# Performance work log

Measured on AMD Instinct MI355X. Metric: run time of the kernel, lower is better.

## Reference

```python
import jax, jax.numpy as jnp
import numpy as np
import math

CHANNELS = 1024
NUM_HEADS = 16
HEAD_DIM = CHANNELS // NUM_HEADS  # 64
ROPE_DIM = int(HEAD_DIM * 0.5)    # 32
BASE_FREQ = 10000.0


def apply_rope(x):
    """x: [b, h, t, d]; rotate first ROPE_DIM features, pass the rest through."""
    t = x.shape[2]
    half = ROPE_DIM // 2
    theta = 1.0 / (BASE_FREQ ** (jnp.arange(0, ROPE_DIM, 2, dtype=jnp.float32) / ROPE_DIM))  # [half]
    ang = jnp.arange(t, dtype=jnp.float32)[:, None] * theta[None, :]  # [t, half]
    ang = jnp.concatenate([ang, ang], axis=-1)  # [t, ROPE_DIM]
    cos = jnp.cos(ang)[None, None, :, :]
    sin = jnp.sin(ang)[None, None, :, :]
    x_rope, x_pass = x[..., :ROPE_DIM], x[..., ROPE_DIM:]
    neg_half = jnp.concatenate([-x_rope[..., half:], x_rope[..., :half]], axis=-1)
    x_rope = x_rope * cos + neg_half * sin
    return jnp.concatenate([x_rope, x_pass], axis=-1)


def proximal_bias(length):
    pos = jnp.arange(length, dtype=jnp.float32)
    diff = pos[None, :] - pos[:, None]
    return -jnp.log1p(jnp.abs(diff))[None, None, :, :]  # [1,1,t,t]


def conv1x1(x, w, b):
    """x: [b, c_in, t], w: [c_out, c_in], b: [c_out] -> [b, c_out, t]"""
    return jnp.einsum('oc,bct->bot', w, x) + b[None, :, None]


def setup_inputs() -> dict:
    key = jax.random.key(0)
    ks = jax.random.split(key, 10)
    B, C, T = 8, CHANNELS, 1024
    scale = 1.0 / math.sqrt(C)
    return {
        "x": jax.random.normal(ks[0], (B, C, T), dtype=jnp.float32),
        "context": jax.random.normal(ks[1], (B, C, T), dtype=jnp.float32),
        "attention_mask": jnp.ones((B, 1, 1, T), dtype=jnp.int32),
        "Wq": jax.random.normal(ks[2], (C, C), dtype=jnp.float32) * scale,
        "bq": jnp.zeros((C,), dtype=jnp.float32),
        "Wk": jax.random.normal(ks[3], (C, C), dtype=jnp.float32) * scale,
        "bk": jnp.zeros((C,), dtype=jnp.float32),
        "Wv": jax.random.normal(ks[4], (C, C), dtype=jnp.float32) * scale,
        "bv": jnp.zeros((C,), dtype=jnp.float32),
        "Wo": jax.random.normal(ks[5], (C, C), dtype=jnp.float32) * scale,
        "bo": jnp.zeros((C,), dtype=jnp.float32),
    }


def reference(x, context, attention_mask, Wq, bq, Wk, bk, Wv, bv, Wo, bo):
    B, C, T = x.shape
    H, D = NUM_HEADS, HEAD_DIM
    q = conv1x1(x, Wq, bq)
    k = conv1x1(context, Wk, bk)
    v = conv1x1(context, Wv, bv)
    # b (h d) t -> b h t d
    def split_heads(z):
        return z.reshape(B, H, D, -1).transpose(0, 1, 3, 2)
    q, k, v = split_heads(q), split_heads(k), split_heads(v)
    q = apply_rope(q)
    k = apply_rope(k)
    scores = jnp.einsum('bhqd,bhkd->bhqk', q, k) / math.sqrt(D)
    scores = scores + proximal_bias(T)  # proximal_bias=True, self-attention
    scores = jnp.where(attention_mask == 0, jnp.float32(-10000.0), scores)
    probs = jax.nn.softmax(scores, axis=-1)  # dropout_rate=0.0 -> identity
    out = jnp.einsum('bhqk,bhkd->bhqd', probs, v)
    # b h q d -> b (h d) q
    out = out.transpose(0, 1, 3, 2).reshape(B, C, T)
    return conv1x1(out, Wo, bo)
```

## Files before the change

kernel.cpp:

```cpp
#include <hip/hip_runtime.h>
#include <hip/hip_bf16.h>
#include <math.h>

#define BB 8
#define CC 1024
#define TT 1024
#define HH 16
#define DD 64

typedef __attribute__((ext_vector_type(8))) short short8;
typedef __attribute__((ext_vector_type(4))) short short4_;
typedef __attribute__((ext_vector_type(4))) float f32x4;

#define QSCALE 0.18033688f

__device__ __forceinline__ unsigned short f2bf(float f) {
    unsigned u = __builtin_bit_cast(unsigned, f);
    u += 0x7fffu + ((u >> 16) & 1u);
    return (unsigned short)(u >> 16);
}

__device__ __forceinline__ f32x4 mfma16(short8 a, short8 b, f32x4 c) {
    return __builtin_amdgcn_mfma_f32_16x16x32_bf16(a, b, c, 0, 0, 0);
}

__device__ __forceinline__ void async16(const void* g, void* l) {
    __builtin_amdgcn_global_load_lds(
        (const __attribute__((address_space(1))) unsigned int*)g,
        (__attribute__((address_space(3))) unsigned int*)l, 16, 0, 0);
}

template<int CTRL>
__device__ __forceinline__ float dpp_mv(float x) {
    return __builtin_bit_cast(float,
        __builtin_amdgcn_update_dpp(0, __builtin_bit_cast(int, x),
                                    CTRL, 0xF, 0xF, false));
}
__device__ __forceinline__ float rowsum16(float x) {
    x += dpp_mv<0xB1>(x);
    x += dpp_mv<0x4E>(x);
    x += dpp_mv<0x141>(x);
    x += dpp_mv<0x140>(x);
    return x;
}

__global__ __launch_bounds__(256) void cast_w_kernel(
    const float* __restrict__ Wq, const float* __restrict__ Wk,
    const float* __restrict__ Wv, const float* __restrict__ Wo,
    unsigned short* __restrict__ dst)
{
    const int z = blockIdx.y;
    const float* W = (z == 0) ? Wq : (z == 1) ? Wk : (z == 2) ? Wv : Wo;
    unsigned short* d = dst + (size_t)z * CC * CC;
    int idx = blockIdx.x * 256 + threadIdx.x;
    float4 f = ((const float4*)W)[idx];
    short4_ s;
    s[0] = (short)f2bf(f.x); s[1] = (short)f2bf(f.y);
    s[2] = (short)f2bf(f.z); s[3] = (short)f2bf(f.w);
    ((short4_*)d)[idx] = s;
}

__global__ __launch_bounds__(256) void tcast2_kernel(
    const float* __restrict__ x, const float* __restrict__ ctx,
    unsigned short* __restrict__ xT, unsigned short* __restrict__ cTo)
{
    __shared__ float sT[64][65];
    const int tid = threadIdx.x;
    const int z = blockIdx.z;
    const float* in = (z < BB) ? x : ctx;
    unsigned short* out = (z < BB) ? xT : cTo;
    const int b = (z < BB) ? z : z - BB;
    const int tB = blockIdx.x * 64, cT = blockIdx.y * 64;

    const float* ib = in + ((size_t)b * CC + cT) * TT + tB;
    const int r = tid >> 2;
    #pragma unroll
    for (int j = 0; j < 4; j++) {
        int t4 = (tid & 3) * 4 + j * 16;
        float4 f = *(const float4*)(ib + (size_t)r * TT + t4);
        sT[r][t4 + 0] = f.x; sT[r][t4 + 1] = f.y;
        sT[r][t4 + 2] = f.z; sT[r][t4 + 3] = f.w;
    }
    __syncthreads();
    const int t_l = tid >> 2, cch = (tid & 3) * 16;
    short8 o0, o1;
    #pragma unroll
    for (int i = 0; i < 8; i++) {
        o0[i] = (short)f2bf(sT[cch + i][t_l]);
        o1[i] = (short)f2bf(sT[cch + 8 + i][t_l]);
    }
    unsigned short* dp = out + ((size_t)b * TT + tB + t_l) * CC + cT + cch;
    *(short8*)dp = o0;
    *(short8*)(dp + 8) = o1;
}

__global__ __launch_bounds__(256) void tcast_kernel(
    const float* __restrict__ in, unsigned short* __restrict__ out)
{
    __shared__ float sT[64][65];
    const int tid = threadIdx.x;
    const int tB = blockIdx.x * 64, cT = blockIdx.y * 64, b = blockIdx.z;

    const float* ib = in + ((size_t)b * CC + cT) * TT + tB;
    const int r = tid >> 2;
    #pragma unroll
    for (int j = 0; j < 4; j++) {
        int t4 = (tid & 3) * 4 + j * 16;
        float4 f = *(const float4*)(ib + (size_t)r * TT + t4);
        sT[r][t4 + 0] = f.x; sT[r][t4 + 1] = f.y;
        sT[r][t4 + 2] = f.z; sT[r][t4 + 3] = f.w;
    }
    __syncthreads();
    const int t_l = tid >> 2, cch = (tid & 3) * 16;
    short8 o0, o1;
    #pragma unroll
    for (int i = 0; i < 8; i++) {
        o0[i] = (short)f2bf(sT[cch + i][t_l]);
        o1[i] = (short)f2bf(sT[cch + 8 + i][t_l]);
    }
    unsigned short* dp = out + ((size_t)b * TT + tB + t_l) * CC + cT + cch;
    *(short8*)dp = o0;
    *(short8*)(dp + 8) = o1;
}

__global__ __launch_bounds__(256) void qkv_gll_kernel(
    const unsigned short* __restrict__ xT, const unsigned short* __restrict__ cT,
    const unsigned short* __restrict__ Wq2, const unsigned short* __restrict__ Wk2,
    const unsigned short* __restrict__ Wv2,
    const float* __restrict__ bq, const float* __restrict__ bk,
    const float* __restrict__ bv,
    unsigned short* __restrict__ qo, unsigned short* __restrict__ ko,
    unsigned short* __restrict__ vo,
    int mode)
{
    __shared__ __align__(16) short smem[4 * 64 * 72];
    short* sA = smem;
    short* sB = smem + 4096;

    const int tid = threadIdx.x, lane = tid & 63, wave = tid >> 6;
    const int wm = wave >> 1, wn = wave & 1;
    const int l15 = lane & 15, lq = lane >> 4;

    const int tTile = blockIdx.x, oTile = blockIdx.y;
    const int zz = blockIdx.z;
    int w, b;
    if (mode == 0)      { w = zz % 3;        b = zz / 3;  }
    else if (mode == 1) { w = 0;             b = zz;      }
    else                { w = 1 + (zz & 1);  b = zz >> 1; }
    const unsigned short* inT = (w == 0) ? xT : cT;
    const int oBase = oTile * 128, tBase = tTile * 128;

    const unsigned short* WA = (w == 0) ? Wq2 : (w == 1) ? Wk2 : Wv2;
    const float* bias        = (w == 0) ? bq  : (w == 1) ? bk  : bv;

    const int srow = lane >> 2;
    const int sch  = (lane ^ (lane >> 2) ^ (lane >> 4)) & 3;
    const unsigned short* gA0 = WA + (size_t)(oBase + wave * 32 + srow) * CC + sch * 8;
    const unsigned short* gA1 = gA0 + (size_t)16 * CC;
    const unsigned short* gB0 = inT + ((size_t)b * TT + tBase + wave * 32 + srow) * CC + sch * 8;
    const unsigned short* gB1 = gB0 + (size_t)16 * CC;
    short* lA0 = sA + (wave * 2 + 0) * 512;
    short* lA1 = sA + (wave * 2 + 1) * 512;
    short* lB0 = sB + (wave * 2 + 0) * 512;
    short* lB1 = sB + (wave * 2 + 1) * 512;

    const int csw = ((lq ^ (l15 & 3) ^ (l15 >> 2)) & 3) * 8;

    f32x4 acc[4][4];
    #pragma unroll
    for (int mt = 0; mt < 4; mt++)
        #pragma unroll
        for (int nt = 0; nt < 4; nt++) acc[mt][nt] = (f32x4){0.f, 0.f, 0.f, 0.f};

    for (int c0 = 0; c0 < CC; c0 += 32) {
        async16(gA0 + c0, lA0);
        async16(gA1 + c0, lA1);
        async16(gB0 + c0, lB0);
        async16(gB1 + c0, lB1);
        __syncthreads();

        short8 af[4], bf[4];
        #pragma unroll
        for (int mt = 0; mt < 4; mt++)
            af[mt] = *(short8*)(sA + (wm * 64 + mt * 16 + l15) * 32 + csw);
        #pragma unroll
        for (int nt = 0; nt < 4; nt++)
            bf[nt] = *(short8*)(sB + (wn * 64 + nt * 16 + l15) * 32 + csw);
        #pragma unroll
        for (int mt = 0; mt < 4; mt++)
            #pragma unroll
            for (int nt = 0; nt < 4; nt++)
                acc[mt][nt] = mfma16(af[mt], bf[nt], acc[mt][nt]);
        __syncthreads();
    }

    #pragma unroll
    for (int mt = 0; mt < 4; mt++)
        #pragma unroll
        for (int r = 0; r < 4; r++) {
            float bi = bias[oBase + wm * 64 + mt * 16 + lq * 4 + r];
            #pragma unroll
            for (int nt = 0; nt < 4; nt++) {
                acc[mt][nt][r] += bi;
                if (w == 0) acc[mt][nt][r] *= QSCALE;
            }
        }

    const int h = oTile * 2 + wm;
    short* sT = smem + wave * (64 * 72);

    if (w < 2) {
        #pragma unroll
        for (int r = 0; r < 4; r++) {
            float dr = (float)(lq * 4 + r);
            float theta = exp2f(dr * -0.8304820237f);
            float sa, ca, ss, cs;
            sincosf((float)(tBase + wn * 64 + l15) * theta, &sa, &ca);
            sincosf(16.0f * theta, &ss, &cs);
            #pragma unroll
            for (int nt = 0; nt < 4; nt++) {
                float x0 = acc[0][nt][r], x1 = acc[1][nt][r];
                acc[0][nt][r] = x0 * ca - x1 * sa;
                acc[1][nt][r] = x1 * ca + x0 * sa;
                float c2 = ca * cs - sa * ss;
                sa = sa * cs + ca * ss;
                ca = c2;
            }
        }
        #pragma unroll
        for (int nt = 0; nt < 4; nt++)
            #pragma unroll
            for (int mt = 0; mt < 4; mt++) {
                short4_ v4;
                #pragma unroll
                for (int r = 0; r < 4; r++) v4[r] = (short)f2bf(acc[mt][nt][r]);
                *(short4_*)(sT + (nt * 16 + l15) * 72 + mt * 16 + lq * 4) = v4;
            }
    } else {
        #pragma unroll
        for (int mt = 0; mt < 4; mt++)
            #pragma unroll
            for (int r = 0; r < 4; r++)
                #pragma unroll
                for (int nt = 0; nt < 4; nt++)
                    sT[(mt * 16 + lq * 4 + r) * 72 + nt * 16 + l15] =
                        (short)f2bf(acc[mt][nt][r]);
    }
    __asm__ volatile("s_waitcnt lgkmcnt(0)" ::: "memory");

    unsigned short* dstBase;
    if (w == 0)
        dstBase = qo + ((size_t)(b * HH + h) * TT + tBase + wn * 64 + lane) * DD;
    else if (w == 1)
        dstBase = ko + ((size_t)(b * HH + h) * TT + tBase + wn * 64 + lane) * DD;
    else
        dstBase = vo + ((size_t)(b * HH + h) * DD + lane) * TT + tBase + wn * 64;
    #pragma unroll
    for (int j = 0; j < 8; j++)
        *(short8*)(dstBase + j * 8) = *(short8*)(sT + lane * 72 + j * 8);
}

__global__ __launch_bounds__(256) void oproj_gll_kernel(
    const unsigned short* __restrict__ att, const unsigned short* __restrict__ Wo2,
    const float* __restrict__ bo, float* __restrict__ out)
{
    __shared__ __align__(16) short smem[8192];
    short* sA = smem;
    short* sB = smem + 4096;

    const int tid = threadIdx.x, lane = tid & 63, wave = tid >> 6;
    const int wm = wave >> 1, wn = wave & 1;
    const int l15 = lane & 15, lq = lane >> 4;
    const int tTile = blockIdx.x, oTile = blockIdx.y, b = blockIdx.z;
    const int oBase = oTile * 128, tBase = tTile * 128;

    const int srow = lane >> 2;
    const int sch  = (lane ^ (lane >> 2) ^ (lane >> 4)) & 3;
    const unsigned short* gA0 = Wo2 + (size_t)(oBase + wave * 32 + srow) * CC + sch * 8;
    const unsigned short* gA1 = gA0 + (size_t)16 * CC;
    const unsigned short* attB = att + (size_t)b * HH * TT * DD;
    const int t0 = tBase + wave * 32 + srow;
    short* lA0 = sA + (wave * 2 + 0) * 512;
    short* lA1 = sA + (wave * 2 + 1) * 512;
    short* lB0 = sB + (wave * 2 + 0) * 512;
    short* lB1 = sB + (wave * 2 + 1) * 512;

    const int csw = ((lq ^ (l15 & 3) ^ (l15 >> 2)) & 3) * 8;

    f32x4 acc[4][4];
    #pragma unroll
    for (int mt = 0; mt < 4; mt++)
        #pragma unroll
        for (int nt = 0; nt < 4; nt++) acc[mt][nt] = (f32x4){0.f, 0.f, 0.f, 0.f};

    for (int c0 = 0; c0 < CC; c0 += 32) {
        int c = c0 + sch * 8;
        const unsigned short* g0 =
            attB + ((size_t)(c >> 6) * TT + t0) * DD + (c & 63);
        async16(gA0 + c0, lA0);
        async16(gA1 + c0, lA1);
        async16(g0, lB0);
        async16(g0 + 16 * DD, lB1);
        __syncthreads();

        short8 af[4], bf[4];
        #pragma unroll
        for (int mt = 0; mt < 4; mt++)
            af[mt] = *(short8*)(sA + (wm * 64 + mt * 16 + l15) * 32 + csw);
        #pragma unroll
        for (int nt = 0; nt < 4; nt++)
            bf[nt] = *(short8*)(sB + (wn * 64 + nt * 16 + l15) * 32 + csw);
        #pragma unroll
        for (int mt = 0; mt < 4; mt++)
            #pragma unroll
            for (int nt = 0; nt < 4; nt++)
                acc[mt][nt] = mfma16(af[mt], bf[nt], acc[mt][nt]);
        __syncthreads();
    }

    #pragma unroll
    for (int mt = 0; mt < 4; mt++)
        #pragma unroll
        for (int r = 0; r < 4; r++) {
            int o = oBase + wm * 64 + mt * 16 + lq * 4 + r;
            float bi = bo[o];
            float* dst = out + ((size_t)b * CC + o) * TT + tBase + wn * 64;
            #pragma unroll
            for (int nt = 0; nt < 4; nt++)
                dst[nt * 16 + l15] = acc[mt][nt][r] + bi;
        }
}

__global__ __launch_bounds__(256) void attn_mfma_kernel(
    const unsigned short* __restrict__ q, const unsigned short* __restrict__ k,
    const unsigned short* __restrict__ v, const int* __restrict__ mask,
    unsigned short* __restrict__ att)
{
    __shared__ __align__(16) short sQw[64 * 72];
    __shared__ __align__(16) short sK[64 * 72];
    __shared__ __align__(16) short sV[64 * 72];
    __shared__ __align__(16) short sP[64 * 72];

    const int tid = threadIdx.x, lane = tid & 63, wq = tid >> 6;
    const int l15 = lane & 15, lq = lane >> 4;
    const int qTile = blockIdx.x, bh = blockIdx.y, b = bh >> 4;

    const int sr = tid >> 2, sc = (tid & 3) * 16;

    {
        const unsigned short* gq = q + ((size_t)bh * TT + qTile * 64 + sr) * DD + sc;
        *(short8*)(sQw + sr * 72 + sc)     = *(const short8*)gq;
        *(short8*)(sQw + sr * 72 + sc + 8) = *(const short8*)(gq + 8);
    }
    __syncthreads();

    const short8 aq0 = *(short8*)(sQw + (wq * 16 + l15) * 72 + lq * 8);
    const short8 aq1 = *(short8*)(sQw + (wq * 16 + l15) * 72 + 32 + lq * 8);
    __syncthreads();

    float* wtab = (float*)sQw;
    #pragma unroll
    for (int j = 0; j < 8; j++) {
        int d = tid + 256 * j;
        int ad = d - 1023; ad = ad < 0 ? -ad : ad;
        wtab[d] = __builtin_amdgcn_rcpf(1.0f + (float)ad);
    }

    f32x4 accO[4];
    float l_acc[4];
    #pragma unroll
    for (int r = 0; r < 4; r++) {
        l_acc[r] = 0.f;
        accO[r] = (f32x4){0.f, 0.f, 0.f, 0.f};
    }

    const int qpos0 = qTile * 64 + wq * 16 + lq * 4;
    const int* maskB = mask + b * TT;
    const unsigned short* kB = k + (size_t)bh * TT * DD;
    const unsigned short* vB = v + (size_t)bh * DD * TT;

    for (int kt = 0; kt < 16; kt++) {
        const unsigned short* gk = kB + (size_t)(kt * 64 + sr) * DD + sc;
        short8 k0 = *(const short8*)gk;
        short8 k1 = *(const short8*)(gk + 8);
        const unsigned short* gv = vB + (size_t)sr * TT + kt * 64 + sc;
        short8 v0 = *(const short8*)gv;
        short8 v1 = *(const short8*)(gv + 8);

        __syncthreads();
        *(short8*)(sK + sr * 72 + sc)     = k0;
        *(short8*)(sK + sr * 72 + sc + 8) = k1;
        *(short8*)(sV + sr * 72 + sc)     = v0;
        *(short8*)(sV + sr * 72 + sc + 8) = v1;
        __syncthreads();

        f32x4 s4[4];
        #pragma unroll
        for (int nt = 0; nt < 4; nt++) {
            short8 b0 = *(short8*)(sK + (nt * 16 + l15) * 72 + lq * 8);
            short8 b1 = *(short8*)(sK + (nt * 16 + l15) * 72 + 32 + lq * 8);
            f32x4 z = (f32x4){0.f, 0.f, 0.f, 0.f};
            z = mfma16(aq0, b0, z);
            z = mfma16(aq1, b1, z);
            s4[nt] = z;
        }

        const float* wrow = wtab + (kt * 64 + l15 - qpos0 + 1020);
        #pragma unroll
        for (int nt = 0; nt < 4; nt++) {
            int kpos = kt * 64 + nt * 16 + l15;
            int mk = maskB[kpos];
            #pragma unroll
            for (int r = 0; r < 4; r++) {
                float pe = exp2f(s4[nt][r]) * wrow[nt * 16 + 3 - r];
                pe = mk ? pe : 0.f;
                l_acc[r] += pe;
                unsigned u = __builtin_bit_cast(unsigned, pe);
                sP[(wq * 16 + lq * 4 + r) * 72 + nt * 16 + l15] =
                    (short)((u + 0x8000u) >> 16);
            }
        }
        __asm__ volatile("s_waitcnt lgkmcnt(0)" ::: "memory");

        short8 ap0 = *(short8*)(sP + (wq * 16 + l15) * 72 + lq * 8);
        short8 ap1 = *(short8*)(sP + (wq * 16 + l15) * 72 + 32 + lq * 8);
        #pragma unroll
        for (int nt = 0; nt < 4; nt++) {
            short8 b0 = *(short8*)(sV + (nt * 16 + l15) * 72 + lq * 8);
            short8 b1 = *(short8*)(sV + (nt * 16 + l15) * 72 + 32 + lq * 8);
            accO[nt] = mfma16(ap0, b0, accO[nt]);
            accO[nt] = mfma16(ap1, b1, accO[nt]);
        }
    }

    unsigned short* aB = att + ((size_t)bh * TT + qTile * 64 + wq * 16 + lq * 4) * DD;
    #pragma unroll
    for (int r = 0; r < 4; r++) {
        float inv = 1.0f / rowsum16(l_acc[r]);
        #pragma unroll
        for (int nt = 0; nt < 4; nt++)
            aB[(size_t)r * DD + nt * 16 + l15] = f2bf(accO[nt][r] * inv);
    }
}

__global__ __launch_bounds__(256) void qkv_mfma_kernel(
    const float* __restrict__ x, const float* __restrict__ ctx,
    const float* __restrict__ Wq, const float* __restrict__ bq,
    const float* __restrict__ Wk, const float* __restrict__ bk,
    const float* __restrict__ Wv, const float* __restrict__ bv,
    unsigned short* __restrict__ qo, unsigned short* __restrict__ ko,
    unsigned short* __restrict__ vo)
{
    __shared__ __align__(16) short smem[4 * 64 * 72];
    short* sA = smem;
    short* sB = smem + 128 * 40;

    const int tid  = threadIdx.x;
    const int lane = tid & 63;
    const int wave = tid >> 6;
    const int wm = wave >> 1, wn = wave & 1;
    const int l15 = lane & 15, lq = lane >> 4;

    const int tTile = blockIdx.x, oTile = blockIdx.y;
    const int b = blockIdx.z / 3, w = blockIdx.z % 3;
    const int oBase = oTile * 128, tBase = tTile * 128;

    const float* In   = (w == 0) ? x  : ctx;
    const float* W    = (w == 0) ? Wq : (w == 1) ? Wk : Wv;
    const float* bias = (w == 0) ? bq : (w == 1) ? bk : bv;
    const float* InB  = In + (size_t)b * CC * TT;

    const int ao = tid >> 1, ak = (tid & 1) * 16;
    const int bt = tid & 127, bk_ = (tid >> 7) * 16;
    const float* gA = W + (size_t)(oBase + ao) * CC + ak;
    const float* gB = InB + (size_t)bk_ * TT + tBase + bt;

    f32x4 acc[4][4];
    #pragma unroll
    for (int mt = 0; mt < 4; mt++)
        #pragma unroll
        for (int nt = 0; nt < 4; nt++) acc[mt][nt] = (f32x4){0.f, 0.f, 0.f, 0.f};

    for (int c0 = 0; c0 < CC; c0 += 32) {
        float fa[16], fb[16];
        #pragma unroll
        for (int i = 0; i < 4; i++) {
            float4 t4 = *(const float4*)(gA + c0 + 4 * i);
            fa[4*i+0] = t4.x; fa[4*i+1] = t4.y; fa[4*i+2] = t4.z; fa[4*i+3] = t4.w;
        }
        #pragma unroll
        for (int j = 0; j < 16; j++)
            fb[j] = gB[(size_t)(c0 + j) * TT];

        __syncthreads();
        short8 pa0, pa1, pb0, pb1;
        #pragma unroll
        for (int e = 0; e < 8; e++) {
            pa0[e] = (short)f2bf(fa[e]);   pa1[e] = (short)f2bf(fa[8 + e]);
            pb0[e] = (short)f2bf(fb[e]);   pb1[e] = (short)f2bf(fb[8 + e]);
        }
        *(short8*)(sA + ao * 40 + ak)     = pa0;
        *(short8*)(sA + ao * 40 + ak + 8) = pa1;
        *(short8*)(sB + bt * 40 + bk_)     = pb0;
        *(short8*)(sB + bt * 40 + bk_ + 8) = pb1;
        __syncthreads();

        short8 af[4], bf[4];
        #pragma unroll
        for (int mt = 0; mt < 4; mt++)
            af[mt] = *(short8*)(sA + (wm * 64 + mt * 16 + l15) * 40 + lq * 8);
        #pragma unroll
        for (int nt = 0; nt < 4; nt++)
            bf[nt] = *(short8*)(sB + (wn * 64 + nt * 16 + l15) * 40 + lq * 8);
        #pragma unroll
        for (int mt = 0; mt < 4; mt++)
            #pragma unroll
            for (int nt = 0; nt < 4; nt++)
                acc[mt][nt] = mfma16(af[mt], bf[nt], acc[mt][nt]);
    }

    #pragma unroll
    for (int mt = 0; mt < 4; mt++)
        #pragma unroll
        for (int r = 0; r < 4; r++) {
            float bi = bias[oBase + wm * 64 + mt * 16 + lq * 4 + r];
            #pragma unroll
            for (int nt = 0; nt < 4; nt++) {
                acc[mt][nt][r] += bi;
                if (w == 0) acc[mt][nt][r] *= QSCALE;
            }
        }

    const int h = oTile * 2 + wm;
    __syncthreads();
    short* sT = smem + wave * (64 * 72);

    if (w < 2) {
        #pragma unroll
        for (int r = 0; r < 4; r++) {
            float theta = powf(10000.0f, -(float)(lq * 4 + r) * (1.0f / 16.0f));
            #pragma unroll
            for (int nt = 0; nt < 4; nt++) {
                float tpos = (float)(tBase + wn * 64 + nt * 16 + l15);
                float sa, ca;
                sincosf(tpos * theta, &sa, &ca);
                float x0 = acc[0][nt][r], x1 = acc[1][nt][r];
                acc[0][nt][r] = x0 * ca - x1 * sa;
                acc[1][nt][r] = x1 * ca + x0 * sa;
            }
        }
        #pragma unroll
        for (int nt = 0; nt < 4; nt++)
            #pragma unroll
            for (int mt = 0; mt < 4; mt++) {
                short4_ v4;
                #pragma unroll
                for (int r = 0; r < 4; r++) v4[r] = (short)f2bf(acc[mt][nt][r]);
                *(short4_*)(sT + (nt * 16 + l15) * 72 + mt * 16 + lq * 4) = v4;
            }
    } else {
        #pragma unroll
        for (int mt = 0; mt < 4; mt++)
            #pragma unroll
            for (int r = 0; r < 4; r++)
                #pragma unroll
                for (int nt = 0; nt < 4; nt++)
                    sT[(mt * 16 + lq * 4 + r) * 72 + nt * 16 + l15] =
                        (short)f2bf(acc[mt][nt][r]);
    }
    __asm__ volatile("s_waitcnt lgkmcnt(0)" ::: "memory");

    unsigned short* dstBase;
    if (w == 0)
        dstBase = qo + ((size_t)(b * HH + h) * TT + tBase + wn * 64 + lane) * DD;
    else if (w == 1)
        dstBase = ko + ((size_t)(b * HH + h) * TT + tBase + wn * 64 + lane) * DD;
    else
        dstBase = vo + ((size_t)(b * HH + h) * DD + lane) * TT + tBase + wn * 64;
    #pragma unroll
    for (int j = 0; j < 8; j++)
        *(short8*)(dstBase + j * 8) = *(short8*)(sT + lane * 72 + j * 8);
}

__global__ __launch_bounds__(256) void oproj_mfma_kernel(
    const unsigned short* __restrict__ att, const float* __restrict__ Wo,
    const float* __restrict__ bo, float* __restrict__ out)
{
    __shared__ __align__(16) short smem[2 * 128 * 40];
    short* sA = smem;
    short* sB = smem + 128 * 40;

    const int tid = threadIdx.x, lane = tid & 63, wave = tid >> 6;
    const int wm = wave >> 1, wn = wave & 1;
    const int l15 = lane & 15, lq = lane >> 4;
    const int tTile = blockIdx.x, oTile = blockIdx.y, b = blockIdx.z;
    const int oBase = oTile * 128, tBase = tTile * 128;

    const int ao = tid >> 1, ak = (tid & 1) * 16;
    const int bt = tid & 127, bk_ = (tid >> 7) * 16;
    const float* gA = Wo + (size_t)(oBase + ao) * CC + ak;

    f32x4 acc[4][4];
    #pragma unroll
    for (int mt = 0; mt < 4; mt++)
        #pragma unroll
        for (int nt = 0; nt < 4; nt++) acc[mt][nt] = (f32x4){0.f, 0.f, 0.f, 0.f};

    for (int c0 = 0; c0 < CC; c0 += 32) {
        float fa[16];
        #pragma unroll
        for (int i = 0; i < 4; i++) {
            float4 t4 = *(const float4*)(gA + c0 + 4 * i);
            fa[4*i+0] = t4.x; fa[4*i+1] = t4.y; fa[4*i+2] = t4.z; fa[4*i+3] = t4.w;
        }
        int c = c0 + bk_;
        const unsigned short* gB =
            att + (((size_t)b * HH + (c >> 6)) * TT + tBase + bt) * DD + (c & 63);
        short8 pb0 = *(const short8*)gB;
        short8 pb1 = *(const short8*)(gB + 8);

        __syncthreads();
        short8 pa0, pa1;
        #pragma unroll
        for (int e = 0; e < 8; e++) {
            pa0[e] = (short)f2bf(fa[e]); pa1[e] = (short)f2bf(fa[8 + e]);
        }
        *(short8*)(sA + ao * 40 + ak)      = pa0;
        *(short8*)(sA + ao * 40 + ak + 8)  = pa1;
        *(short8*)(sB + bt * 40 + bk_)     = pb0;
        *(short8*)(sB + bt * 40 + bk_ + 8) = pb1;
        __syncthreads();

        short8 af[4], bf[4];
        #pragma unroll
        for (int mt = 0; mt < 4; mt++)
            af[mt] = *(short8*)(sA + (wm * 64 + mt * 16 + l15) * 40 + lq * 8);
        #pragma unroll
        for (int nt = 0; nt < 4; nt++)
            bf[nt] = *(short8*)(sB + (wn * 64 + nt * 16 + l15) * 40 + lq * 8);
        #pragma unroll
        for (int mt = 0; mt < 4; mt++)
            #pragma unroll
            for (int nt = 0; nt < 4; nt++)
                acc[mt][nt] = mfma16(af[mt], bf[nt], acc[mt][nt]);
    }

    #pragma unroll
    for (int mt = 0; mt < 4; mt++)
        #pragma unroll
        for (int r = 0; r < 4; r++) {
            int o = oBase + wm * 64 + mt * 16 + lq * 4 + r;
            float bi = bo[o];
            float* dst = out + ((size_t)b * CC + o) * TT + tBase + wn * 64;
            #pragma unroll
            for (int nt = 0; nt < 4; nt++)
                dst[nt * 16 + l15] = acc[mt][nt][r] + bi;
        }
}

extern "C" void kernel_launch(void* const* d_in, const int* in_sizes, int n_in,
                              void* d_out, int out_size, void* d_ws, size_t ws_size,
                              hipStream_t stream)
{
    const float* x   = (const float*)d_in[0];
    const float* ctx = (const float*)d_in[1];
    const int* mask  = (const int*)d_in[2];
    const float* Wq  = (const float*)d_in[3];
    const float* bq  = (const float*)d_in[4];
    const float* Wk  = (const float*)d_in[5];
    const float* bk  = (const float*)d_in[6];
    const float* Wv  = (const float*)d_in[7];
    const float* bv  = (const float*)d_in[8];
    const float* Wo  = (const float*)d_in[9];
    const float* bo  = (const float*)d_in[10];
    float* out = (float*)d_out;

    const size_t nq = (size_t)BB * HH * TT * DD;
    const size_t nw = (size_t)CC * CC;

    if (ws_size >= (5 * nq + 4 * nw) * sizeof(unsigned short)) {
        unsigned short* q   = (unsigned short*)d_ws;
        unsigned short* k   = q + nq;
        unsigned short* v   = k + nq;
        unsigned short* xT  = v + nq;
        unsigned short* cT  = xT + nq;
        unsigned short* Wb  = cT + nq;
        unsigned short* Wqb = Wb;
        unsigned short* Wkb = Wb + nw;
        unsigned short* Wvb = Wb + 2 * nw;
        unsigned short* Wob = Wb + 3 * nw;

        cast_w_kernel<<<dim3(1024, 4), 256, 0, stream>>>(Wq, Wk, Wv, Wo, Wb);
        tcast2_kernel<<<dim3(16, 16, BB * 2), 256, 0, stream>>>(x, ctx, xT, cT);
        qkv_gll_kernel<<<dim3(8, 8, BB * 3), 256, 0, stream>>>(
            xT, cT, Wqb, Wkb, Wvb, bq, bk, bv, q, k, v, 0);
        attn_mfma_kernel<<<dim3(TT / 64, BB * HH), 256, 0, stream>>>(
            q, k, v, mask, xT);
        oproj_gll_kernel<<<dim3(8, 8, BB), 256, 0, stream>>>(xT, Wob, bo, out);
    } else if (ws_size >= (4 * nq + 4 * nw) * sizeof(unsigned short)) {
        unsigned short* q   = (unsigned short*)d_ws;
        unsigned short* k   = q + nq;
        unsigned short* v   = k + nq;
        unsigned short* buf = v + nq;
        unsigned short* Wb  = buf + nq;
        unsigned short* Wqb = Wb;
        unsigned short* Wkb = Wb + nw;
        unsigned short* Wvb = Wb + 2 * nw;
        unsigned short* Wob = Wb + 3 * nw;

        cast_w_kernel<<<dim3(1024, 4), 256, 0, stream>>>(Wq, Wk, Wv, Wo, Wb);
        tcast_kernel<<<dim3(16, 16, BB), 256, 0, stream>>>(x, buf);
        qkv_gll_kernel<<<dim3(8, 8, BB), 256, 0, stream>>>(
            buf, buf, Wqb, Wkb, Wvb, bq, bk, bv, q, k, v, 1);
        tcast_kernel<<<dim3(16, 16, BB), 256, 0, stream>>>(ctx, buf);
        qkv_gll_kernel<<<dim3(8, 8, BB * 2), 256, 0, stream>>>(
            buf, buf, Wqb, Wkb, Wvb, bq, bk, bv, q, k, v, 2);
        attn_mfma_kernel<<<dim3(TT / 64, BB * HH), 256, 0, stream>>>(
            q, k, v, mask, buf);
        oproj_gll_kernel<<<dim3(8, 8, BB), 256, 0, stream>>>(buf, Wob, bo, out);
    } else {
        unsigned short* q   = (unsigned short*)d_ws;
        unsigned short* k   = q + nq;
        unsigned short* v   = k + nq;
        unsigned short* att = v + nq;
        qkv_mfma_kernel<<<dim3(8, 8, BB * 3), 256, 0, stream>>>(
            x, ctx, Wq, bq, Wk, bk, Wv, bv, q, k, v);
        attn_mfma_kernel<<<dim3(TT / 64, BB * HH), 256, 0, stream>>>(
            q, k, v, mask, att);
        oproj_mfma_kernel<<<dim3(8, 8, BB), 256, 0, stream>>>(att, Wo, bo, out);
    }
}
```

Baseline: 339.3 us.

## Compute S transposed to keep P in registers and prefetch next K/V tile

```diff
diff --git a/kernel.cpp b/kernel.cpp
--- a/kernel.cpp
+++ b/kernel.cpp
@@ -11,6 +11,8 @@
 typedef __attribute__((ext_vector_type(8))) short short8;
 typedef __attribute__((ext_vector_type(4))) short short4_;
 typedef __attribute__((ext_vector_type(4))) float f32x4;
+typedef __attribute__((ext_vector_type(4))) int   i32x4;
+typedef __attribute__((ext_vector_type(2))) unsigned long long u64x2;
 
 #define QSCALE 0.18033688f
 
@@ -30,18 +32,17 @@
         (__attribute__((address_space(3))) unsigned int*)l, 16, 0, 0);
 }
 
-template<int CTRL>
-__device__ __forceinline__ float dpp_mv(float x) {
-    return __builtin_bit_cast(float,
-        __builtin_amdgcn_update_dpp(0, __builtin_bit_cast(int, x),
-                                    CTRL, 0xF, 0xF, false));
-}
-__device__ __forceinline__ float rowsum16(float x) {
-    x += dpp_mv<0xB1>(x);
-    x += dpp_mv<0x4E>(x);
-    x += dpp_mv<0x141>(x);
-    x += dpp_mv<0x140>(x);
-    return x;
+__device__ __forceinline__ unsigned cvtpk(float lo, float hi) {
+    unsigned r;
+    asm("v_cvt_pk_bf16_f32 %0, %1, %2" : "=v"(r) : "v"(lo), "v"(hi));
+    return r;
+}
+
+__device__ __forceinline__ short8 vfrag(const short* p) {
+    u64x2 t;
+    t[0] = *(const unsigned long long*)(p);
+    t[1] = *(const unsigned long long*)(p + 16);
+    return __builtin_bit_cast(short8, t);
 }
 
 __global__ __launch_bounds__(256) void cast_w_kernel(
@@ -339,7 +340,6 @@
     __shared__ __align__(16) short sQw[64 * 72];
     __shared__ __align__(16) short sK[64 * 72];
     __shared__ __align__(16) short sV[64 * 72];
-    __shared__ __align__(16) short sP[64 * 72];
 
     const int tid = threadIdx.x, lane = tid & 63, wq = tid >> 6;
     const int l15 = lane & 15, lq = lane >> 4;
@@ -354,8 +354,8 @@
     }
     __syncthreads();
 
-    const short8 aq0 = *(short8*)(sQw + (wq * 16 + l15) * 72 + lq * 8);
-    const short8 aq1 = *(short8*)(sQw + (wq * 16 + l15) * 72 + 32 + lq * 8);
+    const short8 bq0 = *(short8*)(sQw + (wq * 16 + l15) * 72 + lq * 8);
+    const short8 bq1 = *(short8*)(sQw + (wq * 16 + l15) * 72 + 32 + lq * 8);
     __syncthreads();
 
     float* wtab = (float*)sQw;
@@ -367,76 +367,89 @@
     }
 
     f32x4 accO[4];
-    float l_acc[4];
-    #pragma unroll
-    for (int r = 0; r < 4; r++) {
-        l_acc[r] = 0.f;
-        accO[r] = (f32x4){0.f, 0.f, 0.f, 0.f};
-    }
-
-    const int qpos0 = qTile * 64 + wq * 16 + lq * 4;
+    #pragma unroll
+    for (int nt = 0; nt < 4; nt++) accO[nt] = (f32x4){0.f, 0.f, 0.f, 0.f};
+    float l_sum = 0.f;
+
+    const int qpos = qTile * 64 + wq * 16 + l15;
     const int* maskB = mask + b * TT;
     const unsigned short* kB = k + (size_t)bh * TT * DD;
     const unsigned short* vB = v + (size_t)bh * DD * TT;
 
+    const unsigned short* gk = kB + (size_t)sr * DD + sc;
+    const unsigned short* gv = vB + (size_t)sr * TT + sc;
+    short8 kr0 = *(const short8*)gk;
+    short8 kr1 = *(const short8*)(gk + 8);
+    short8 vr0 = *(const short8*)gv;
+    short8 vr1 = *(const short8*)(gv + 8);
+
     for (int kt = 0; kt < 16; kt++) {
-        const unsigned short* gk = kB + (size_t)(kt * 64 + sr) * DD + sc;
-        short8 k0 = *(const short8*)gk;
-        short8 k1 = *(const short8*)(gk + 8);
-        const unsigned short* gv = vB + (size_t)sr * TT + kt * 64 + sc;
-        short8 v0 = *(const short8*)gv;
-        short8 v1 = *(const short8*)(gv + 8);
-
-        __syncthreads();
-        *(short8*)(sK + sr * 72 + sc)     = k0;
-        *(short8*)(sK + sr * 72 + sc + 8) = k1;
-        *(short8*)(sV + sr * 72 + sc)     = v0;
-        *(short8*)(sV + sr * 72 + sc + 8) = v1;
-        __syncthreads();
+        __syncthreads();
+        *(short8*)(sK + sr * 72 + sc)     = kr0;
+        *(short8*)(sK + sr * 72 + sc + 8) = kr1;
+        *(short8*)(sV + sr * 72 + sc)     = vr0;
+        *(short8*)(sV + sr * 72 + sc + 8) = vr1;
+        __syncthreads();
+
+        if (kt < 15) {
+            gk += 64 * DD;
+            gv += 64;
+            kr0 = *(const short8*)gk;
+            kr1 = *(const short8*)(gk + 8);
+            vr0 = *(const short8*)gv;
+            vr1 = *(const short8*)(gv + 8);
+        }
 
         f32x4 s4[4];
         #pragma unroll
         for (int nt = 0; nt < 4; nt++) {
-            short8 b0 = *(short8*)(sK + (nt * 16 + l15) * 72 + lq * 8);
-            short8 b1 = *(short8*)(sK + (nt * 16 + l15) * 72 + 32 + lq * 8);
+            short8 ka0 = *(short8*)(sK + (nt * 16 + l15) * 72 + lq * 8);
+            short8 ka1 = *(short8*)(sK + (nt * 16 + l15) * 72 + 32 + lq * 8);
             f32x4 z = (f32x4){0.f, 0.f, 0.f, 0.f};
-            z = mfma16(aq0, b0, z);
-            z = mfma16(aq1, b1, z);
+            z = mfma16(ka0, bq0, z);
+            z = mfma16(ka1, bq1, z);
             s4[nt] = z;
         }
 
-        const float* wrow = wtab + (kt * 64 + l15 - qpos0 + 1020);
+        const float* wrow = wtab + (kt * 64 + lq * 4 + 1023 - qpos);
+        unsigned pk8[4][2];
         #pragma unroll
         for (int nt = 0; nt < 4; nt++) {
-            int kpos = kt * 64 + nt * 16 + l15;
-            int mk = maskB[kpos];
-            #pragma unroll
-            for (int r = 0; r < 4; r++) {
-                float pe = exp2f(s4[nt][r]) * wrow[nt * 16 + 3 - r];
-                pe = mk ? pe : 0.f;
-                l_acc[r] += pe;
-                unsigned u = __builtin_bit_cast(unsigned, pe);
-                sP[(wq * 16 + lq * 4 + r) * 72 + nt * 16 + l15] =
-                    (short)((u + 0x8000u) >> 16);
+            i32x4 mk = *(const i32x4*)(maskB + kt * 64 + nt * 16 + lq * 4);
+            #pragma unroll
+            for (int h2 = 0; h2 < 2; h2++) {
+                float p0 = exp2f(s4[nt][2 * h2])     * wrow[nt * 16 + 2 * h2];
+                float p1 = exp2f(s4[nt][2 * h2 + 1]) * wrow[nt * 16 + 2 * h2 + 1];
+                p0 = mk[2 * h2]     ? p0 : 0.f;
+                p1 = mk[2 * h2 + 1] ? p1 : 0.f;
+                l_sum += p0 + p1;
+                pk8[nt][h2] = cvtpk(p0, p1);
             }
         }
-        __asm__ volatile("s_waitcnt lgkmcnt(0)" ::: "memory");
-
-        short8 ap0 = *(short8*)(sP + (wq * 16 + l15) * 72 + lq * 8);
-        short8 ap1 = *(short8*)(sP + (wq * 16 + l15) * 72 + 32 + lq * 8);
+
+        i32x4 c0 = {(int)pk8[0][0], (int)pk8[0][1], (int)pk8[1][0], (int)pk8[1][1]};
+        i32x4 c1 = {(int)pk8[2][0], (int)pk8[2][1], (int)pk8[3][0], (int)pk8[3][1]};
+        short8 ap0 = __builtin_bit_cast(short8, c0);
+        short8 ap1 = __builtin_bit_cast(short8, c1);
+
         #pragma unroll
         for (int nt = 0; nt < 4; nt++) {
-            short8 b0 = *(short8*)(sV + (nt * 16 + l15) * 72 + lq * 8);
-            short8 b1 = *(short8*)(sV + (nt * 16 + l15) * 72 + 32 + lq * 8);
+            const short* vr = sV + (nt * 16 + l15) * 72 + lq * 4;
+            short8 b0 = vfrag(vr);
+            short8 b1 = vfrag(vr + 32);
             accO[nt] = mfma16(ap0, b0, accO[nt]);
             accO[nt] = mfma16(ap1, b1, accO[nt]);
         }
     }
 
+    float tot = l_sum;
+    tot += __shfl_xor(tot, 16);
+    tot += __shfl_xor(tot, 32);
+
     unsigned short* aB = att + ((size_t)bh * TT + qTile * 64 + wq * 16 + lq * 4) * DD;
     #pragma unroll
     for (int r = 0; r < 4; r++) {
-        float inv = 1.0f / rowsum16(l_acc[r]);
+        float inv = 1.0f / __shfl(tot, lq * 4 + r);
         #pragma unroll
         for (int nt = 0; nt < 4; nt++)
             aB[(size_t)r * DD + nt * 16 + l15] = f2bf(accO[nt][r] * inv);
```

Result: faster. 330.0 us (-2.8%).
